# Performance work log

Hardware: AMD Instinct MI355X
Metric: run time of the kernel (lower is better)

## Reference

```python
import jax, jax.numpy as jnp
import numpy as np

N = 8192       # node_number
D = 64         # embed_dim
S = 4096       # number of triad samples
BETA0 = 0.1
BETA1 = 0.1
MARGIN = 1.0
EPS = 1e-6
P_EDGE = 0.004  # edge density -> avg degree ~33


def setup_inputs() -> dict:
    key = jax.random.key(0)
    k1, k2, k3, k4, k5, k6, k7, k8, k9, k10 = jax.random.split(key, 10)
    emb_t = jax.random.normal(k1, (N, D), dtype=jnp.float32) * 0.05
    emb_prev = jax.random.normal(k2, (N, D), dtype=jnp.float32) * 0.05
    theta = jax.random.normal(k3, (N, D), dtype=jnp.float32) * 0.05
    edge_mask = jax.random.uniform(k4, (N, N)) < P_EDGE
    adj = jnp.where(edge_mask, jax.random.uniform(k5, (N, N), dtype=jnp.float32), 0.0)
    j_idx = jax.random.randint(k6, (S,), 0, N, dtype=jnp.int32)
    k_idx = jax.random.randint(k7, (S,), 0, N, dtype=jnp.int32)
    negj_idx = jax.random.randint(k8, (S,), 0, N, dtype=jnp.int32)
    i_idx = jax.random.randint(k9, (S,), 0, N, dtype=jnp.int32)
    condition = jax.random.randint(k10, (S,), -1, 2, dtype=jnp.int32)  # {-1,0,1}
    return {
        "emb_t": emb_t, "emb_prev": emb_prev, "theta": theta, "adj": adj,
        "j_idx": j_idx, "k_idx": k_idx, "negj_idx": negj_idx,
        "i_idx": i_idx, "condition": condition,
    }


def _loss(emb_t, emb_prev, theta, adj, j_idx, k_idx, negj_idx, i_idx, condition):
    E = emb_t
    # ---- L_sh: triplet hinge, per sample ----
    uj, uk, unj = E[j_idx], E[k_idx], E[negj_idx]          # [S, D]
    pos = jnp.sum((uj - uk) ** 2, axis=-1)                  # [S]
    neg = jnp.sum((unj - uk) ** 2, axis=-1)                 # [S]
    L_sh = jnp.sum(jax.nn.relu(pos - neg + MARGIN))
    # ---- L_tr: common-neighbor closure loss ----
    # dot(s, l) = theta_l . x(i,j,l) where x = adj[i,l]*(u_l-u_i) + adj[j,l]*(u_l-u_j)
    Ai = adj[i_idx]                                         # [S, N] gather of adj rows
    Aj = adj[j_idx]                                         # [S, N]
    diag = jnp.sum(theta * E, axis=-1)                      # [N]  theta_l . u_l
    ui = E[i_idx]                                           # [S, D]
    ti = ui @ theta.T                                       # [S, N]  theta_l . u_i
    tj = uj @ theta.T                                       # [S, N]  theta_l . u_j
    dots = Ai * (diag[None, :] - ti) + Aj * (diag[None, :] - tj)  # [S, N]
    # P = sigmoid(dot), with the original power>100 cutoff (power = -dot)
    P_all = jnp.where(dots < -100.0, 0.0, jax.nn.sigmoid(dots))
    cn_mask = (Ai > 0) & (Aj > 0)                           # common neighbors of (i, j)
    C1 = 1.0 - jnp.prod(jnp.where(cn_mask, 1.0 - P_all, 1.0), axis=1)  # [S]
    dot_k = jnp.take_along_axis(dots, k_idx[:, None].astype(jnp.int32), axis=1)[:, 0]  # [S]
    C0 = jnp.where(dot_k < -100.0, 0.0, jax.nn.sigmoid(dot_k))
    C = 1.0 - C0 / (C1 + EPS)
    log_p = jax.nn.softplus(-dot_k)                         # log(1 + exp(-theta_k.x))
    vest = jnp.where(condition == 1, C, dot_k)
    ltr = jnp.where(condition == -1, 0.0, log_p + vest)
    L_tr = jnp.sum(ltr)
    # ---- L_smooth: added once per sample (timestamp strictly between 0 and graph_number) ----
    n_samples = jnp.float32(j_idx.shape[0])
    L_smooth = n_samples * jnp.sum((emb_t - emb_prev) ** 2)
    return L_sh + BETA0 * L_tr + BETA1 * L_smooth


def reference(emb_t, emb_prev, theta, adj, j_idx, k_idx, negj_idx, i_idx, condition):
    return _loss(emb_t, emb_prev, theta, adj, j_idx, k_idx, negj_idx, i_idx, condition)
```

## Files before the change

kernel.cpp:

```cpp
#include <hip/hip_runtime.h>
#include <math.h>

#define NN 8192
#define DD 64
#define SS 4096
#define BETA0 0.1
#define BETA1 0.1


__global__ void init_acc_kernel(double* acc) {
    if (threadIdx.x < 4) acc[threadIdx.x] = 0.0;
}

__global__ void diag_kernel(const float* __restrict__ E,
                            const float* __restrict__ theta,
                            float* __restrict__ diag) {
    int gid  = blockIdx.x * blockDim.x + threadIdx.x;
    int row  = gid >> 6;
    int lane = gid & 63;
    if (row < NN) {
        float v = theta[(size_t)row * DD + lane] * E[(size_t)row * DD + lane];
        #pragma unroll
        for (int o = 32; o; o >>= 1) v += __shfl_down(v, o);
        if (lane == 0) diag[row] = v;
    }
}

__global__ void smooth_kernel(const float4* __restrict__ a,
                              const float4* __restrict__ b,
                              double* __restrict__ acc) {
    const int total = NN * DD / 4;
    int idx = blockIdx.x * blockDim.x + threadIdx.x;
    float sum = 0.f;
    for (int t = idx; t < total; t += gridDim.x * blockDim.x) {
        float4 x = a[t], y = b[t];
        float d0 = x.x - y.x, d1 = x.y - y.y, d2 = x.z - y.z, d3 = x.w - y.w;
        sum += d0 * d0 + d1 * d1 + d2 * d2 + d3 * d3;
    }
    #pragma unroll
    for (int o = 32; o; o >>= 1) sum += __shfl_down(sum, o);
    __shared__ float wsum[4];
    int lane = threadIdx.x & 63, wv = threadIdx.x >> 6;
    if (lane == 0) wsum[wv] = sum;
    __syncthreads();
    if (threadIdx.x == 0)
        atomicAdd(&acc[2], (double)(wsum[0] + wsum[1] + wsum[2] + wsum[3]));
}

__global__ void __launch_bounds__(256) sample_kernel(
        const float* __restrict__ E, const float* __restrict__ theta,
        const float* __restrict__ adj, const float* __restrict__ diag,
        const int* __restrict__ j_idx, const int* __restrict__ k_idx,
        const int* __restrict__ nj_idx, const int* __restrict__ i_idx,
        const int* __restrict__ cond, double* __restrict__ acc) {
    int s   = blockIdx.x;
    int tid = threadIdx.x;
    int j = j_idx[s], k = k_idx[s], nj = nj_idx[s], i = i_idx[s], c = cond[s];

    __shared__ float ui_sh[DD], uj_sh[DD];
    __shared__ float sc[4];
    __shared__ float wprod[4];

    if (tid < DD) {
        float ui_ = E[(size_t)i * DD + tid];
        float uj_ = E[(size_t)j * DD + tid];
        ui_sh[tid] = ui_;
        uj_sh[tid] = uj_;
        float uk_ = E[(size_t)k * DD + tid];
        float un_ = E[(size_t)nj * DD + tid];
        float thk = theta[(size_t)k * DD + tid];
        float dp = uj_ - uk_, dn = un_ - uk_;
        float pos = dp * dp, neg = dn * dn;
        float tik = thk * ui_, tjk = thk * uj_;
        #pragma unroll
        for (int o = 32; o; o >>= 1) {
            pos += __shfl_down(pos, o);
            neg += __shfl_down(neg, o);
            tik += __shfl_down(tik, o);
            tjk += __shfl_down(tjk, o);
        }
        if (tid == 0) { sc[0] = pos; sc[1] = neg; sc[2] = tik; sc[3] = tjk; }
    }
    __syncthreads();

    float prodAll = 1.0f;
    if (c == 1) {
        float prod = 1.0f;
        const float4* ri = (const float4*)(adj + (size_t)i * NN);
        const float4* rj = (const float4*)(adj + (size_t)j * NN);
        for (int b = tid; b < NN / 4; b += 256) {
            float4 a4 = ri[b];
            float4 b4 = rj[b];
            float ai[4] = {a4.x, a4.y, a4.z, a4.w};
            float aj[4] = {b4.x, b4.y, b4.z, b4.w};
            #pragma unroll
            for (int q = 0; q < 4; q++) {
                if (ai[q] > 0.f && aj[q] > 0.f) {
                    int l = b * 4 + q;
                    const float* th = theta + (size_t)l * DD;
                    float til = 0.f, tjl = 0.f;
                    for (int d = 0; d < DD; d++) {
                        float t = th[d];
                        til = fmaf(t, ui_sh[d], til);
                        tjl = fmaf(t, uj_sh[d], tjl);
                    }
                    float dg = diag[l];
                    float dl = ai[q] * (dg - til) + aj[q] * (dg - tjl);
                    float P = (dl < -100.f) ? 0.f : 1.f / (1.f + expf(-dl));
                    prod *= (1.f - P);
                }
            }
        }
        #pragma unroll
        for (int o = 32; o; o >>= 1) prod *= __shfl_down(prod, o);
        int lane = tid & 63, wv = tid >> 6;
        if (lane == 0) wprod[wv] = prod;
        __syncthreads();
        if (tid == 0) prodAll = wprod[0] * wprod[1] * wprod[2] * wprod[3];
    }

    if (tid == 0) {
        float pos = sc[0], neg = sc[1], tik = sc[2], tjk = sc[3];
        float lsh = fmaxf(pos - neg + 1.0f, 0.f);

        float aik = adj[(size_t)i * NN + k];
        float ajk = adj[(size_t)j * NN + k];
        float dgk = diag[k];
        float dot_k = aik * (dgk - tik) + ajk * (dgk - tjk);

        float x = -dot_k;
        float logp = fmaxf(x, 0.f) + log1pf(expf(-fabsf(x)));

        float ltr;
        if (c == -1) {
            ltr = 0.f;
        } else if (c == 0) {
            ltr = logp + dot_k;
        } else {
            float C1 = 1.f - prodAll;
            float C0 = (dot_k < -100.f) ? 0.f : 1.f / (1.f + expf(-dot_k));
            ltr = logp + (1.f - C0 / (C1 + 1e-6f));
        }
        atomicAdd(&acc[0], (double)lsh);
        atomicAdd(&acc[1], (double)ltr);
    }
}

__global__ void final_kernel(const double* __restrict__ acc,
                             float* __restrict__ out) {
    if (blockIdx.x == 0 && threadIdx.x == 0) {
        double loss = acc[0] + BETA0 * acc[1] + BETA1 * (double)SS * acc[2];
        out[0] = (float)loss;
    }
}

extern "C" void kernel_launch(void* const* d_in, const int* in_sizes, int n_in,
                              void* d_out, int out_size, void* d_ws, size_t ws_size,
                              hipStream_t stream) {
    const float* emb_t    = (const float*)d_in[0];
    const float* emb_prev = (const float*)d_in[1];
    const float* theta    = (const float*)d_in[2];
    const float* adj      = (const float*)d_in[3];
    const int*   j_idx    = (const int*)d_in[4];
    const int*   k_idx    = (const int*)d_in[5];
    const int*   nj_idx   = (const int*)d_in[6];
    const int*   i_idx    = (const int*)d_in[7];
    const int*   cond     = (const int*)d_in[8];
    float* out = (float*)d_out;

    double* acc  = (double*)d_ws;
    float*  diag = (float*)(acc + 4);

    init_acc_kernel<<<1, 64, 0, stream>>>(acc);
    diag_kernel<<<(NN * 64) / 256, 256, 0, stream>>>(emb_t, theta, diag);
    smooth_kernel<<<256, 256, 0, stream>>>((const float4*)emb_t,
                                           (const float4*)emb_prev, acc);
    sample_kernel<<<SS, 256, 0, stream>>>(emb_t, theta, adj, diag,
                                          j_idx, k_idx, nj_idx, i_idx, cond, acc);
    final_kernel<<<1, 64, 0, stream>>>(acc, out);
}
```

Baseline: 416.5 us.

## Map one sample per wavefront with ballot-driven common-neighbor processing and fused reductions

Each wavefront now handles one sample instead of one block per sample. Common neighbors are found with a ballot and each one is processed cooperatively across the 64 lanes using a shuffle reduction, replacing the old serial per-thread 64-long dot product. The diag, smooth and init kernels are folded into the sample kernel by computing diag on the fly and taking one row of the smooth term per sample. Per-sample partials are written to a buffer and summed in a single final reduction kernel instead of using double atomics. The catch is that every common neighbor costs several cross-lane reductions, and block-level parallelism per sample drops.

```diff
diff --git a/kernel.cpp b/kernel.cpp
--- a/kernel.cpp
+++ b/kernel.cpp
@@ -4,128 +4,84 @@
 #define NN 8192
 #define DD 64
 #define SS 4096
-#define BETA0 0.1
-#define BETA1 0.1
 
-
-__global__ void init_acc_kernel(double* acc) {
-    if (threadIdx.x < 4) acc[threadIdx.x] = 0.0;
+__device__ __forceinline__ float wred(float v) {
+    #pragma unroll
+    for (int o = 1; o < 64; o <<= 1) v += __shfl_xor(v, o);
+    return v;
 }
 
-__global__ void diag_kernel(const float* __restrict__ E,
-                            const float* __restrict__ theta,
-                            float* __restrict__ diag) {
-    int gid  = blockIdx.x * blockDim.x + threadIdx.x;
-    int row  = gid >> 6;
-    int lane = gid & 63;
-    if (row < NN) {
-        float v = theta[(size_t)row * DD + lane] * E[(size_t)row * DD + lane];
-        #pragma unroll
-        for (int o = 32; o; o >>= 1) v += __shfl_down(v, o);
-        if (lane == 0) diag[row] = v;
-    }
-}
-
-__global__ void smooth_kernel(const float4* __restrict__ a,
-                              const float4* __restrict__ b,
-                              double* __restrict__ acc) {
-    const int total = NN * DD / 4;
-    int idx = blockIdx.x * blockDim.x + threadIdx.x;
-    float sum = 0.f;
-    for (int t = idx; t < total; t += gridDim.x * blockDim.x) {
-        float4 x = a[t], y = b[t];
-        float d0 = x.x - y.x, d1 = x.y - y.y, d2 = x.z - y.z, d3 = x.w - y.w;
-        sum += d0 * d0 + d1 * d1 + d2 * d2 + d3 * d3;
-    }
-    #pragma unroll
-    for (int o = 32; o; o >>= 1) sum += __shfl_down(sum, o);
-    __shared__ float wsum[4];
-    int lane = threadIdx.x & 63, wv = threadIdx.x >> 6;
-    if (lane == 0) wsum[wv] = sum;
-    __syncthreads();
-    if (threadIdx.x == 0)
-        atomicAdd(&acc[2], (double)(wsum[0] + wsum[1] + wsum[2] + wsum[3]));
-}
-
-__global__ void __launch_bounds__(256) sample_kernel(
-        const float* __restrict__ E, const float* __restrict__ theta,
-        const float* __restrict__ adj, const float* __restrict__ diag,
+__global__ void __launch_bounds__(256) fused_sample_kernel(
+        const float* __restrict__ E, const float* __restrict__ Eprev,
+        const float* __restrict__ theta, const float* __restrict__ adj,
         const int* __restrict__ j_idx, const int* __restrict__ k_idx,
         const int* __restrict__ nj_idx, const int* __restrict__ i_idx,
-        const int* __restrict__ cond, double* __restrict__ acc) {
-    int s   = blockIdx.x;
-    int tid = threadIdx.x;
+        const int* __restrict__ cond, float4* __restrict__ part) {
+    int wave = threadIdx.x >> 6;
+    int lane = threadIdx.x & 63;
+    int s = blockIdx.x * 4 + wave;
+
     int j = j_idx[s], k = k_idx[s], nj = nj_idx[s], i = i_idx[s], c = cond[s];
 
-    __shared__ float ui_sh[DD], uj_sh[DD];
-    __shared__ float sc[4];
-    __shared__ float wprod[4];
+    float ui  = E[(size_t)i  * DD + lane];
+    float uj  = E[(size_t)j  * DD + lane];
+    float uk  = E[(size_t)k  * DD + lane];
+    float un  = E[(size_t)nj * DD + lane];
+    float thk = theta[(size_t)k * DD + lane];
 
-    if (tid < DD) {
-        float ui_ = E[(size_t)i * DD + tid];
-        float uj_ = E[(size_t)j * DD + tid];
-        ui_sh[tid] = ui_;
-        uj_sh[tid] = uj_;
-        float uk_ = E[(size_t)k * DD + tid];
-        float un_ = E[(size_t)nj * DD + tid];
-        float thk = theta[(size_t)k * DD + tid];
-        float dp = uj_ - uk_, dn = un_ - uk_;
-        float pos = dp * dp, neg = dn * dn;
-        float tik = thk * ui_, tjk = thk * uj_;
-        #pragma unroll
-        for (int o = 32; o; o >>= 1) {
-            pos += __shfl_down(pos, o);
-            neg += __shfl_down(neg, o);
-            tik += __shfl_down(tik, o);
-            tjk += __shfl_down(tjk, o);
-        }
-        if (tid == 0) { sc[0] = pos; sc[1] = neg; sc[2] = tik; sc[3] = tjk; }
+    float dp = uj - uk, dn = un - uk;
+    float pos = wred(dp * dp);
+    float neg = wred(dn * dn);
+    float tik = wred(thk * ui);
+    float tjk = wred(thk * uj);
+    float dgk = wred(thk * uk);
+
+    float sm;
+    {
+        const float2* a2 = (const float2*)E;
+        const float2* b2 = (const float2*)Eprev;
+        float2 x = a2[(size_t)s * 64 + lane];
+        float2 y = b2[(size_t)s * 64 + lane];
+        float dx = x.x - y.x, dy = x.y - y.y;
+        sm = wred(dx * dx + dy * dy);
     }
-    __syncthreads();
 
-    float prodAll = 1.0f;
+    float prod = 1.0f;
     if (c == 1) {
-        float prod = 1.0f;
         const float4* ri = (const float4*)(adj + (size_t)i * NN);
         const float4* rj = (const float4*)(adj + (size_t)j * NN);
-        for (int b = tid; b < NN / 4; b += 256) {
-            float4 a4 = ri[b];
-            float4 b4 = rj[b];
-            float ai[4] = {a4.x, a4.y, a4.z, a4.w};
-            float aj[4] = {b4.x, b4.y, b4.z, b4.w};
+        #pragma unroll 2
+        for (int it = 0; it < NN / 4 / 64; ++it) {
+            float4 a4 = ri[it * 64 + lane];
+            float4 b4 = rj[it * 64 + lane];
+            float av[4] = {a4.x, a4.y, a4.z, a4.w};
+            float bv[4] = {b4.x, b4.y, b4.z, b4.w};
             #pragma unroll
-            for (int q = 0; q < 4; q++) {
-                if (ai[q] > 0.f && aj[q] > 0.f) {
-                    int l = b * 4 + q;
-                    const float* th = theta + (size_t)l * DD;
-                    float til = 0.f, tjl = 0.f;
-                    for (int d = 0; d < DD; d++) {
-                        float t = th[d];
-                        til = fmaf(t, ui_sh[d], til);
-                        tjl = fmaf(t, uj_sh[d], tjl);
-                    }
-                    float dg = diag[l];
-                    float dl = ai[q] * (dg - til) + aj[q] * (dg - tjl);
-                    float P = (dl < -100.f) ? 0.f : 1.f / (1.f + expf(-dl));
+            for (int q = 0; q < 4; ++q) {
+                unsigned long long m = __ballot(av[q] > 0.f && bv[q] > 0.f);
+                while (m) {
+                    int src = __ffsll((long long)m) - 1;
+                    m &= m - 1;
+                    float ai = __shfl(av[q], src);
+                    float aj = __shfl(bv[q], src);
+                    int l = (it * 64 + src) * 4 + q;
+                    float th = theta[(size_t)l * DD + lane];
+                    float ul = E[(size_t)l * DD + lane];
+                    float r1 = wred(th * (ul - ui));
+                    float r2 = wred(th * (ul - uj));
+                    float dl = ai * r1 + aj * r2;
+                    float P = (dl < -100.f) ? 0.f : 1.f / (1.f + __expf(-dl));
                     prod *= (1.f - P);
                 }
             }
         }
-        #pragma unroll
-        for (int o = 32; o; o >>= 1) prod *= __shfl_down(prod, o);
-        int lane = tid & 63, wv = tid >> 6;
-        if (lane == 0) wprod[wv] = prod;
-        __syncthreads();
-        if (tid == 0) prodAll = wprod[0] * wprod[1] * wprod[2] * wprod[3];
     }
 
-    if (tid == 0) {
-        float pos = sc[0], neg = sc[1], tik = sc[2], tjk = sc[3];
+    if (lane == 0) {
         float lsh = fmaxf(pos - neg + 1.0f, 0.f);
 
         float aik = adj[(size_t)i * NN + k];
         float ajk = adj[(size_t)j * NN + k];
-        float dgk = diag[k];
         float dot_k = aik * (dgk - tik) + ajk * (dgk - tjk);
 
         float x = -dot_k;
@@ -137,20 +93,38 @@
         } else if (c == 0) {
             ltr = logp + dot_k;
         } else {
-            float C1 = 1.f - prodAll;
+            float C1 = 1.f - prod;
             float C0 = (dot_k < -100.f) ? 0.f : 1.f / (1.f + expf(-dot_k));
             ltr = logp + (1.f - C0 / (C1 + 1e-6f));
         }
-        atomicAdd(&acc[0], (double)lsh);
-        atomicAdd(&acc[1], (double)ltr);
+        part[s] = make_float4(lsh, ltr, sm, 0.f);
     }
 }
 
-__global__ void final_kernel(const double* __restrict__ acc,
-                             float* __restrict__ out) {
-    if (blockIdx.x == 0 && threadIdx.x == 0) {
-        double loss = acc[0] + BETA0 * acc[1] + BETA1 * (double)SS * acc[2];
-        out[0] = (float)loss;
+__global__ void __launch_bounds__(256) final_reduce_kernel(
+        const float4* __restrict__ part, float* __restrict__ out) {
+    double lsh = 0.0, ltr = 0.0, sm = 0.0;
+    for (int t = threadIdx.x; t < SS; t += 256) {
+        float4 p = part[t];
+        lsh += (double)p.x;
+        ltr += (double)p.y;
+        sm  += (double)p.z;
+    }
+    #pragma unroll
+    for (int o = 32; o; o >>= 1) {
+        lsh += __shfl_down(lsh, o);
+        ltr += __shfl_down(ltr, o);
+        sm  += __shfl_down(sm, o);
+    }
+    __shared__ double sh[3][4];
+    int lane = threadIdx.x & 63, wv = threadIdx.x >> 6;
+    if (lane == 0) { sh[0][wv] = lsh; sh[1][wv] = ltr; sh[2][wv] = sm; }
+    __syncthreads();
+    if (threadIdx.x == 0) {
+        double L = (sh[0][0] + sh[0][1] + sh[0][2] + sh[0][3])
+                 + 0.1 * (sh[1][0] + sh[1][1] + sh[1][2] + sh[1][3])
+                 + 0.1 * (double)SS * (sh[2][0] + sh[2][1] + sh[2][2] + sh[2][3]);
+        out[0] = (float)L;
     }
 }
 
@@ -168,14 +142,9 @@
     const int*   cond     = (const int*)d_in[8];
     float* out = (float*)d_out;
 
-    double* acc  = (double*)d_ws;
-    float*  diag = (float*)(acc + 4);
+    float4* part = (float4*)d_ws;
 
-    init_acc_kernel<<<1, 64, 0, stream>>>(acc);
-    diag_kernel<<<(NN * 64) / 256, 256, 0, stream>>>(emb_t, theta, diag);
-    smooth_kernel<<<256, 256, 0, stream>>>((const float4*)emb_t,
-                                           (const float4*)emb_prev, acc);
-    sample_kernel<<<SS, 256, 0, stream>>>(emb_t, theta, adj, diag,
-                                          j_idx, k_idx, nj_idx, i_idx, cond, acc);
-    final_kernel<<<1, 64, 0, stream>>>(acc, out);
+    fused_sample_kernel<<<SS / 4, 256, 0, stream>>>(
+        emb_t, emb_prev, theta, adj, j_idx, k_idx, nj_idx, i_idx, cond, part);
+    final_reduce_kernel<<<1, 256, 0, stream>>>(part, out);
 }
```

After: 341.3 us. -18.1%, faster.
